# Performance work log

Measured on AMD Instinct MI355X. Metric: run time of the kernel, lower is better.

## Reference

```python
import jax, jax.numpy as jnp
import numpy as np

POLY_DEGREE = 2
LEVELS = 3


def setup_inputs() -> dict:
    key = jax.random.key(0)
    B, T, C = 32, 4096, 128
    x = jax.random.normal(key, (B, T, C), dtype=jnp.float32)
    return {"x": x}


def reference(x):
    B, T, C = x.shape
    t = jnp.linspace(0.0, 1.0, T, dtype=x.dtype)[:, None]          # [T,1]
    Tmat = jnp.concatenate([t ** i for i in range(POLY_DEGREE + 1)], axis=1)  # [T,d+1]
    # Least-squares solution is identical across batch & channel since the
    # design matrix is shared: sol = pinv(Tmat) @ x  (closed-form, one solve).
    P = jnp.linalg.pinv(Tmat)                                       # [d+1,T]
    coef = jnp.einsum('dt,btc->bdc', P, x)                          # [B,d+1,C]
    low = jnp.einsum('td,bdc->btc', Tmat, coef)                     # [B,T,C] trend
    res = x - low                                                   # residual
    highs = [res] + [jnp.zeros_like(res) for _ in range(LEVELS - 1)]
    return (low, highs)
```

## Files before the change

kernel.cpp:

```cpp
#include <hip/hip_runtime.h>

typedef float f4 __attribute__((ext_vector_type(4)));

#define TT 4096
#define CC 128
#define BB 32
#define NG 64
#define C4 (CC / 4)
#define ROWS_G (TT / NG)

__global__ __launch_bounds__(256) void k_moments(const f4* __restrict__ x4,
                                                 f4* __restrict__ partial,
                                                 float scale) {
    const int blk = blockIdx.x;
    const int b = blk >> 6;
    const int g = blk & 63;
    const int tid = threadIdx.x;
    const int r = tid >> 5;
    const int q = tid & 31;
    const f4* xb = x4 + (size_t)b * TT * C4;
    const int t0 = g * ROWS_G;

    f4 m0 = (f4)0.0f, m1 = (f4)0.0f, m2 = (f4)0.0f;
#pragma unroll
    for (int k = 0; k < 8; ++k) {
        const int t = t0 + r + (k << 3);
        const float u = fmaf((float)t, scale, -0.5f);
        const f4 v = xb[(size_t)t * C4 + q];
        m0 += v;
        m1 += u * v;
        m2 += (u * u) * v;
    }

    __shared__ f4 red[3][8][32];
    red[0][r][q] = m0;
    red[1][r][q] = m1;
    red[2][r][q] = m2;
    __syncthreads();

    if (tid < 32) {
#pragma unroll
        for (int j = 0; j < 3; ++j) {
            f4 s = red[j][0][tid];
#pragma unroll
            for (int rr = 1; rr < 8; ++rr) s += red[j][rr][tid];
            partial[(size_t)blk * (3 * C4) + j * C4 + tid] = s;
        }
    }
}

template <bool FUSE_ZERO>
__global__ __launch_bounds__(256) void k_emit(const f4* __restrict__ x4,
                                              const f4* __restrict__ partial,
                                              f4* __restrict__ out,
                                              float scale, float c20,
                                              float invS0, float invS2,
                                              float invD) {
    const size_t N4 = (size_t)BB * TT * C4;
    const int blk = blockIdx.x;
    const int b = blk >> 6;
    const int g = blk & 63;
    const int tid = threadIdx.x;
    const int r = tid >> 5;
    const int q = tid & 31;

    __shared__ f4 red[3][8][32];
    __shared__ f4 ca[3][32];

    const f4* pb = partial + (size_t)b * (64 * 3 * C4);
#pragma unroll
    for (int j = 0; j < 3; ++j) {
        f4 acc = (f4)0.0f;
#pragma unroll
        for (int k = 0; k < 8; ++k)
            acc += pb[(size_t)(r + (k << 3)) * (3 * C4) + j * C4 + q];
        red[j][r][q] = acc;
    }
    __syncthreads();
    if (tid < 32) {
        f4 s0 = (f4)0.0f, s1 = (f4)0.0f, s2 = (f4)0.0f;
#pragma unroll
        for (int rr = 0; rr < 8; ++rr) {
            s0 += red[0][rr][tid];
            s1 += red[1][rr][tid];
            s2 += red[2][rr][tid];
        }
        ca[0][tid] = s0 * invS0;
        ca[1][tid] = s1 * invS2;
        ca[2][tid] = (s2 - c20 * s0) * invD;
    }
    __syncthreads();

    const f4 a0 = ca[0][q];
    const f4 a1 = ca[1][q];
    const f4 a2 = ca[2][q];
    const f4 z = (f4)0.0f;

    const size_t base = (size_t)b * TT * C4;
    const int t0 = g * ROWS_G;
#pragma unroll
    for (int k = 0; k < 8; ++k) {
        const int t = t0 + r + (k << 3);
        const float u = fmaf((float)t, scale, -0.5f);
        const float w = fmaf(u, u, -c20);
        const size_t idx = base + (size_t)t * C4 + q;
        const f4 xv = x4[idx];
        const f4 lo = a0 + u * a1 + w * a2;
        const f4 re = xv - lo;
        __builtin_nontemporal_store(lo, &out[idx]);
        __builtin_nontemporal_store(re, &out[N4 + idx]);
        if (FUSE_ZERO) {
            __builtin_nontemporal_store(z, &out[2 * N4 + idx]);
            __builtin_nontemporal_store(z, &out[3 * N4 + idx]);
        }
    }
}

extern "C" void kernel_launch(void* const* d_in, const int* in_sizes, int n_in,
                              void* d_out, int out_size, void* d_ws, size_t ws_size,
                              hipStream_t stream) {
    const float* x = (const float*)d_in[0];
    float* out = (float*)d_out;
    const size_t N = (size_t)BB * TT * CC;

    double S0 = (double)TT, S2 = 0.0, S4 = 0.0;
    for (int i = 0; i < TT; ++i) {
        double u = (double)i / (double)(TT - 1) - 0.5;
        double u2 = u * u;
        S2 += u2;
        S4 += u2 * u2;
    }
    const double c20d = S2 / S0;
    const double Dd = S4 - S2 * S2 / S0;
    const float scale = (float)(1.0 / (double)(TT - 1));
    const float invS0 = (float)(1.0 / S0);
    const float invS2 = (float)(1.0 / S2);
    const float invD  = (float)(1.0 / Dd);
    const float c20   = (float)c20d;

    const size_t partial_elems = (size_t)BB * NG * 3 * C4;
    const size_t need_bytes    = partial_elems * sizeof(f4);

    if (ws_size >= need_bytes) {
        f4* partial = (f4*)d_ws;
        k_moments<<<BB * NG, 256, 0, stream>>>((const f4*)x, partial, scale);
        k_emit<true><<<BB * NG, 256, 0, stream>>>((const f4*)x, partial,
                                                  (f4*)out, scale, c20,
                                                  invS0, invS2, invD);
    } else {
        f4* partial = (f4*)(out + 2 * N);
        k_moments<<<BB * NG, 256, 0, stream>>>((const f4*)x, partial, scale);
        k_emit<false><<<BB * NG, 256, 0, stream>>>((const f4*)x, partial,
                                                   (f4*)out, scale, c20,
                                                   invS0, invS2, invD);
        hipMemsetAsync(out + 2 * N, 0, 2 * N * sizeof(float), stream);
    }
}
```

Measured before the change: 63.74 us.

## Move zero-fill of extra outputs into moments kernel and coarsen moment slabs

The moments pass now uses 16 slabs of 256 rows per batch instead of 64 slabs of 64 rows, which cuts the partial-sum count that the emit kernel must re-reduce. The zeroing of the two all-zero output levels moves from the emit kernel into extra blocks of the moments launch. The write-heavy zeroing can then overlap with the read-bound moment reduction and make the emit kernel lighter. A separate moments-only kernel covers the fallback path.

```diff
diff --git a/kernel.cpp b/kernel.cpp
--- a/kernel.cpp
+++ b/kernel.cpp
@@ -5,46 +5,64 @@
 #define TT 4096
 #define CC 128
 #define BB 32
-#define NG 64
 #define C4 (CC / 4)
-#define ROWS_G (TT / NG)
-
-__global__ __launch_bounds__(256) void k_moments(const f4* __restrict__ x4,
-                                                 f4* __restrict__ partial,
-                                                 float scale) {
+#define NGM 16
+#define SLAB (TT / NGM)
+#define NTILE 64
+
+__global__ __launch_bounds__(256) void k_moments_zero(const f4* __restrict__ x4,
+                                                      f4* __restrict__ partial,
+                                                      f4* __restrict__ out,
+                                                      float scale) {
+    const size_t N4 = (size_t)BB * TT * C4;
     const int blk = blockIdx.x;
-    const int b = blk >> 6;
-    const int g = blk & 63;
     const int tid = threadIdx.x;
     const int r = tid >> 5;
     const int q = tid & 31;
-    const f4* xb = x4 + (size_t)b * TT * C4;
-    const int t0 = g * ROWS_G;
-
-    f4 m0 = (f4)0.0f, m1 = (f4)0.0f, m2 = (f4)0.0f;
-#pragma unroll
-    for (int k = 0; k < 8; ++k) {
-        const int t = t0 + r + (k << 3);
-        const float u = fmaf((float)t, scale, -0.5f);
-        const f4 v = xb[(size_t)t * C4 + q];
-        m0 += v;
-        m1 += u * v;
-        m2 += (u * u) * v;
-    }
-
-    __shared__ f4 red[3][8][32];
-    red[0][r][q] = m0;
-    red[1][r][q] = m1;
-    red[2][r][q] = m2;
-    __syncthreads();
-
-    if (tid < 32) {
-#pragma unroll
-        for (int j = 0; j < 3; ++j) {
-            f4 s = red[j][0][tid];
-#pragma unroll
-            for (int rr = 1; rr < 8; ++rr) s += red[j][rr][tid];
-            partial[(size_t)blk * (3 * C4) + j * C4 + tid] = s;
+
+    if (blk < BB * NGM) {
+        const int b = blk >> 4;
+        const int s = blk & 15;
+        const f4* xb = x4 + (size_t)b * TT * C4;
+        const int t0 = s * SLAB;
+
+        f4 m0 = (f4)0.0f, m1 = (f4)0.0f, m2 = (f4)0.0f;
+#pragma unroll 8
+        for (int k = 0; k < SLAB / 8; ++k) {
+            const int t = t0 + r + (k << 3);
+            const float u = fmaf((float)t, scale, -0.5f);
+            const f4 v = xb[(size_t)t * C4 + q];
+            m0 += v;
+            m1 += u * v;
+            m2 += (u * u) * v;
+        }
+
+        __shared__ f4 red[3][8][32];
+        red[0][r][q] = m0;
+        red[1][r][q] = m1;
+        red[2][r][q] = m2;
+        __syncthreads();
+
+        if (tid < 32) {
+#pragma unroll
+            for (int j = 0; j < 3; ++j) {
+                f4 acc = red[j][0][tid];
+#pragma unroll
+                for (int rr = 1; rr < 8; ++rr) acc += red[j][rr][tid];
+                partial[(size_t)blk * (3 * C4) + j * C4 + tid] = acc;
+            }
+        }
+    } else {
+        const int zid = blk - BB * NGM;
+        const int b = zid >> 6;
+        const int tile = zid & 63;
+        const size_t base = (size_t)b * TT * C4 + (size_t)(tile * 64) * C4;
+        const f4 z = (f4)0.0f;
+#pragma unroll
+        for (int k = 0; k < 8; ++k) {
+            const size_t idx = base + (size_t)(r + (k << 3)) * C4 + q;
+            __builtin_nontemporal_store(z, &out[2 * N4 + idx]);
+            __builtin_nontemporal_store(z, &out[3 * N4 + idx]);
         }
     }
 }
@@ -59,7 +77,7 @@
     const size_t N4 = (size_t)BB * TT * C4;
     const int blk = blockIdx.x;
     const int b = blk >> 6;
-    const int g = blk & 63;
+    const int tile = blk & 63;
     const int tid = threadIdx.x;
     const int r = tid >> 5;
     const int q = tid & 31;
@@ -67,14 +85,12 @@
     __shared__ f4 red[3][8][32];
     __shared__ f4 ca[3][32];
 
-    const f4* pb = partial + (size_t)b * (64 * 3 * C4);
+    const f4* pb = partial + (size_t)b * (NGM * 3 * C4);
 #pragma unroll
     for (int j = 0; j < 3; ++j) {
-        f4 acc = (f4)0.0f;
-#pragma unroll
-        for (int k = 0; k < 8; ++k)
-            acc += pb[(size_t)(r + (k << 3)) * (3 * C4) + j * C4 + q];
-        red[j][r][q] = acc;
+        const f4 e0 = pb[(size_t)(2 * r + 0) * (3 * C4) + j * C4 + q];
+        const f4 e1 = pb[(size_t)(2 * r + 1) * (3 * C4) + j * C4 + q];
+        red[j][r][q] = e0 + e1;
     }
     __syncthreads();
     if (tid < 32) {
@@ -97,7 +113,7 @@
     const f4 z = (f4)0.0f;
 
     const size_t base = (size_t)b * TT * C4;
-    const int t0 = g * ROWS_G;
+    const int t0 = tile * 64;
 #pragma unroll
     for (int k = 0; k < 8; ++k) {
         const int t = t0 + r + (k << 3);
@@ -116,6 +132,46 @@
     }
 }
 
+__global__ __launch_bounds__(256) void k_moments_only(const f4* __restrict__ x4,
+                                                      f4* __restrict__ partial,
+                                                      float scale) {
+    const int blk = blockIdx.x;
+    const int tid = threadIdx.x;
+    const int r = tid >> 5;
+    const int q = tid & 31;
+    const int b = blk >> 4;
+    const int s = blk & 15;
+    const f4* xb = x4 + (size_t)b * TT * C4;
+    const int t0 = s * SLAB;
+
+    f4 m0 = (f4)0.0f, m1 = (f4)0.0f, m2 = (f4)0.0f;
+#pragma unroll 8
+    for (int k = 0; k < SLAB / 8; ++k) {
+        const int t = t0 + r + (k << 3);
+        const float u = fmaf((float)t, scale, -0.5f);
+        const f4 v = xb[(size_t)t * C4 + q];
+        m0 += v;
+        m1 += u * v;
+        m2 += (u * u) * v;
+    }
+
+    __shared__ f4 red[3][8][32];
+    red[0][r][q] = m0;
+    red[1][r][q] = m1;
+    red[2][r][q] = m2;
+    __syncthreads();
+
+    if (tid < 32) {
+#pragma unroll
+        for (int j = 0; j < 3; ++j) {
+            f4 acc = red[j][0][tid];
+#pragma unroll
+            for (int rr = 1; rr < 8; ++rr) acc += red[j][rr][tid];
+            partial[(size_t)blk * (3 * C4) + j * C4 + tid] = acc;
+        }
+    }
+}
+
 extern "C" void kernel_launch(void* const* d_in, const int* in_sizes, int n_in,
                               void* d_out, int out_size, void* d_ws, size_t ws_size,
                               hipStream_t stream) {
@@ -138,21 +194,21 @@
     const float invD  = (float)(1.0 / Dd);
     const float c20   = (float)c20d;
 
-    const size_t partial_elems = (size_t)BB * NG * 3 * C4;
+    const size_t partial_elems = (size_t)BB * NGM * 3 * C4;
     const size_t need_bytes    = partial_elems * sizeof(f4);
 
     if (ws_size >= need_bytes) {
         f4* partial = (f4*)d_ws;
-        k_moments<<<BB * NG, 256, 0, stream>>>((const f4*)x, partial, scale);
-        k_emit<true><<<BB * NG, 256, 0, stream>>>((const f4*)x, partial,
-                                                  (f4*)out, scale, c20,
-                                                  invS0, invS2, invD);
+        k_moments_zero<<<BB * NGM + BB * NTILE, 256, 0, stream>>>(
+            (const f4*)x, partial, (f4*)out, scale);
+        k_emit<false><<<BB * NTILE, 256, 0, stream>>>(
+            (const f4*)x, partial, (f4*)out, scale, c20, invS0, invS2, invD);
     } else {
         f4* partial = (f4*)(out + 2 * N);
-        k_moments<<<BB * NG, 256, 0, stream>>>((const f4*)x, partial, scale);
-        k_emit<false><<<BB * NG, 256, 0, stream>>>((const f4*)x, partial,
-                                                   (f4*)out, scale, c20,
-                                                   invS0, invS2, invD);
+        k_moments_only<<<BB * NGM, 256, 0, stream>>>((const f4*)x, partial,
+                                                     scale);
+        k_emit<false><<<BB * NTILE, 256, 0, stream>>>(
+            (const f4*)x, partial, (f4*)out, scale, c20, invS0, invS2, invD);
         hipMemsetAsync(out + 2 * N, 0, 2 * N * sizeof(float), stream);
     }
 }
```

Measured after the change: 61.68 us. 3.2% less time.
